# Performance work log

Hardware: AMD Instinct MI355X
Metric: run time of the kernel (lower is better)

## Reference

```python
import jax, jax.numpy as jnp
import numpy as np

IN_FEATURES = 4096
OUT_FEATURES = 4096
ACTIVE_IN = 1024
ACTIVE_OUT = 1024
BATCH, SEQ = 4, 2048


def setup_inputs() -> dict:
    key = jax.random.key(0)
    kx, kw, kb = jax.random.split(key, 3)
    x = jax.random.normal(kx, (BATCH, SEQ, IN_FEATURES), dtype=jnp.float32)
    # nn.Linear default init scale ~ 1/sqrt(fan_in)
    W = jax.random.normal(kw, (ACTIVE_OUT, ACTIVE_IN), dtype=jnp.float32) / np.sqrt(ACTIVE_IN)
    b = jax.random.normal(kb, (ACTIVE_OUT,), dtype=jnp.float32) / np.sqrt(ACTIVE_IN)
    rng = np.random.default_rng(42)
    # unique sorted index subsets (faithful to pruning-style selection; scatter is write-once)
    in_idx = jnp.asarray(np.sort(rng.choice(IN_FEATURES, ACTIVE_IN, replace=False)), dtype=jnp.int32)
    out_idx = jnp.asarray(np.sort(rng.choice(OUT_FEATURES, ACTIVE_OUT, replace=False)), dtype=jnp.int32)
    return {"x": x, "W": W, "b": b, "in_idx": in_idx, "out_idx": out_idx}


def reference(x, W, b, in_idx, out_idx):
    # gather active input columns: [B, S, ACTIVE_IN]
    x_active = jnp.take(x, in_idx, axis=-1)
    # dense linear: y = x_active @ W.T + b -> [B, S, ACTIVE_OUT]
    y = jnp.einsum('bsi,oi->bso', x_active, W) + b
    # scatter into zero-initialized full output buffer: [B, S, OUT_FEATURES]
    out = jnp.zeros(x.shape[:-1] + (OUT_FEATURES,), dtype=y.dtype)
    out = out.at[..., out_idx].set(y)
    return out
```

## Files before the change

### kernel.cpp

```cpp
#include <hip/hip_runtime.h>
#include <hip/hip_bf16.h>


typedef unsigned short u16;
typedef u16   u16x4 __attribute__((ext_vector_type(4)));
typedef int   i32x4 __attribute__((ext_vector_type(4)));
typedef float f32x4 __attribute__((ext_vector_type(4)));
typedef __bf16 bf16x8 __attribute__((ext_vector_type(8)));

constexpr int IN_F  = 4096;
constexpr int OUT_F = 4096;
constexpr int AI    = 1024;
constexpr int AO    = 1024;
constexpr int M_ROWS = 4 * 2048;
constexpr int NT_K  = AI / 64;

__device__ __forceinline__ u16 f2bf(float f) {
    union { __hip_bfloat16 h; u16 u; } cv;
    cv.h = __float2bfloat16(f);
    return cv.u;
}

__global__ void prep_kernel(const float* __restrict__ W,
                            const int* __restrict__ out_idx,
                            u16* __restrict__ Wb, int* __restrict__ pos) {
    int t = blockIdx.x * blockDim.x + threadIdx.x;
    if (t < AO) pos[out_idx[t]] = t;
    f32x4 w = reinterpret_cast<const f32x4*>(W)[t];
    u16x4 v;
    v.x = f2bf(w.x); v.y = f2bf(w.y); v.z = f2bf(w.z); v.w = f2bf(w.w);
    reinterpret_cast<u16x4*>(Wb)[t] = v;
}

__global__ __launch_bounds__(256)
void gather_kernel(const float* __restrict__ x,
                   const int* __restrict__ in_idx,
                   u16* __restrict__ Xa) {
    __shared__ float xrow[IN_F];
    const int m = blockIdx.x;
    const int t = threadIdx.x;
    const f32x4* src = reinterpret_cast<const f32x4*>(x + (size_t)m * IN_F);
#pragma unroll
    for (int i = 0; i < 4; ++i)
        *reinterpret_cast<f32x4*>(&xrow[i * 1024 + t * 4]) = src[i * 256 + t];
    __syncthreads();
    i32x4 idx = reinterpret_cast<const i32x4*>(in_idx)[t];
    u16x4 v;
    v.x = f2bf(xrow[idx.x]);
    v.y = f2bf(xrow[idx.y]);
    v.z = f2bf(xrow[idx.z]);
    v.w = f2bf(xrow[idx.w]);
    reinterpret_cast<u16x4*>(Xa + (size_t)m * AI)[t] = v;
}

template <bool PRE>
__global__ __launch_bounds__(256, 2)
void gemm128(const float* __restrict__ x, const u16* __restrict__ Xa,
             const u16* __restrict__ Wb, const float* __restrict__ bias,
             const int* __restrict__ in_idx, float* __restrict__ out) {
    __shared__ u16 As[2][128 * 64];
    __shared__ u16 Bs[2][128 * 64];
    const int tid  = threadIdx.x;
    const int wid  = tid >> 6;
    const int lane = tid & 63;
    const int n_lo = lane & 15;
    const int kg   = lane >> 4;
    const int orig = blockIdx.x;
    const int wgid = (orig & 7) * 64 + (orig >> 3);
    const int mb = wgid >> 3, nb = wgid & 7;
    const int m0 = mb * 128, n0 = nb * 128;
    const int wm = wid >> 1, wn = wid & 1;

    auto stage = [&](int buf, int k0) {
        if constexpr (PRE) {
            const int r8 = lane >> 3;
            const int c8 = (lane & 7) * 8;
#pragma unroll
            for (int c = 0; c < 4; ++c) {
                const int row = wid * 32 + c * 8;
                __builtin_amdgcn_global_load_lds(
                    (const __attribute__((address_space(1))) void*)
                        (Xa + (size_t)(m0 + row + r8) * AI + k0 + c8),
                    (__attribute__((address_space(3))) void*)&As[buf][row * 64],
                    16, 0, 0);
                __builtin_amdgcn_global_load_lds(
                    (const __attribute__((address_space(1))) void*)
                        (Wb + (size_t)(n0 + row + r8) * AI + k0 + c8),
                    (__attribute__((address_space(3))) void*)&Bs[buf][row * 64],
                    16, 0, 0);
            }
        } else {
            const int rr = tid >> 1;
            const int cc = (tid & 1) * 32;
#pragma unroll
            for (int j4 = 0; j4 < 32; j4 += 4) {
                u16x4 va;
#pragma unroll
                for (int j = 0; j < 4; ++j)
                    va[j] = f2bf(x[(size_t)(m0 + rr) * IN_F + in_idx[k0 + cc + j4 + j]]);
                *reinterpret_cast<u16x4*>(&As[buf][rr * 64 + cc + j4]) = va;
                *reinterpret_cast<u16x4*>(&Bs[buf][rr * 64 + cc + j4]) =
                    *reinterpret_cast<const u16x4*>(Wb + (size_t)(n0 + rr) * AI + k0 + cc + j4);
            }
        }
    };

    f32x4 acc[4][4];
#pragma unroll
    for (int i = 0; i < 4; ++i)
#pragma unroll
        for (int j = 0; j < 4; ++j) acc[i][j] = (f32x4)0.0f;

    stage(0, 0);
    int buf = 0;
    for (int kt = 0; kt < NT_K; ++kt) {
        __syncthreads();
        if (kt + 1 < NT_K) stage(buf ^ 1, (kt + 1) * 64);
#pragma unroll
        for (int kk = 0; kk < 64; kk += 32) {
            bf16x8 a[4], b[4];
#pragma unroll
            for (int i = 0; i < 4; ++i)
                a[i] = *reinterpret_cast<const bf16x8*>(
                    &As[buf][(wm * 64 + i * 16 + n_lo) * 64 + kk + kg * 8]);
#pragma unroll
            for (int j = 0; j < 4; ++j)
                b[j] = *reinterpret_cast<const bf16x8*>(
                    &Bs[buf][(wn * 64 + j * 16 + n_lo) * 64 + kk + kg * 8]);
#pragma unroll
            for (int i = 0; i < 4; ++i)
#pragma unroll
                for (int j = 0; j < 4; ++j)
                    acc[i][j] = __builtin_amdgcn_mfma_f32_16x16x32_bf16(
                        a[i], b[j], acc[i][j], 0, 0, 0);
        }
        buf ^= 1;
    }

    float bv[4];
#pragma unroll
    for (int j = 0; j < 4; ++j) bv[j] = bias[n0 + wn * 64 + j * 16 + n_lo];
#pragma unroll
    for (int i = 0; i < 4; ++i) {
        const int gm = m0 + wm * 64 + i * 16 + kg * 4;
#pragma unroll
        for (int j = 0; j < 4; ++j) {
            const int gn = n0 + wn * 64 + j * 16 + n_lo;
#pragma unroll
            for (int r = 0; r < 4; ++r)
                out[(size_t)(gm + r) * OUT_F + gn] = acc[i][j][r] + bv[j];
        }
    }
}

__global__ __launch_bounds__(256)
void expand_kernel(const int* __restrict__ pos, float* __restrict__ out) {
    __shared__ float yrow[AO];
    const int m = blockIdx.x;
    const int t = threadIdx.x;
    float* row = out + (size_t)m * OUT_F;
    *reinterpret_cast<f32x4*>(&yrow[t * 4]) =
        *reinterpret_cast<const f32x4*>(row + t * 4);
    __syncthreads();
    const i32x4* pos4 = reinterpret_cast<const i32x4*>(pos);
#pragma unroll
    for (int c = 0; c < 4; ++c) {
        const int o4 = c * 256 + t;
        i32x4 p = pos4[o4];
        f32x4 v;
        v.x = (p.x >= 0) ? yrow[p.x] : 0.0f;
        v.y = (p.y >= 0) ? yrow[p.y] : 0.0f;
        v.z = (p.z >= 0) ? yrow[p.z] : 0.0f;
        v.w = (p.w >= 0) ? yrow[p.w] : 0.0f;
        *reinterpret_cast<f32x4*>(row + o4 * 4) = v;
    }
}

extern "C" void kernel_launch(void* const* d_in, const int* in_sizes, int n_in,
                              void* d_out, int out_size, void* d_ws, size_t ws_size,
                              hipStream_t stream) {
    const float* x      = (const float*)d_in[0];
    const float* W      = (const float*)d_in[1];
    const float* b      = (const float*)d_in[2];
    const int*   in_idx = (const int*)d_in[3];
    const int*   out_idx= (const int*)d_in[4];
    float* out = (float*)d_out;

    char* ws = (char*)d_ws;
    int* pos = (int*)ws;
    u16* Wb  = (u16*)(ws + 16384);
    u16* Xa  = (u16*)(ws + 16384 + 2 * 1024 * 1024);
    const size_t NEED_FULL = 16384 + 2u * 1024 * 1024 + (size_t)M_ROWS * AI * 2;

    hipMemsetAsync(pos, 0xFF, OUT_F * sizeof(int), stream);
    prep_kernel<<<1024, 256, 0, stream>>>(W, out_idx, Wb, pos);

    if (ws_size >= NEED_FULL) {
        gather_kernel<<<M_ROWS, 256, 0, stream>>>(x, in_idx, Xa);
        gemm128<true><<<(M_ROWS / 128) * (AO / 128), 256, 0, stream>>>(
            x, Xa, Wb, b, in_idx, out);
    } else {
        gemm128<false><<<(M_ROWS / 128) * (AO / 128), 256, 0, stream>>>(
            x, Xa, Wb, b, in_idx, out);
    }
    expand_kernel<<<M_ROWS, 256, 0, stream>>>(pos, out);
}
```

Measured before the change: 281.6 us.

## Fuse scatter-expand into GEMM epilogue via shared-memory staging

Removes the separate expand kernel. Each GEMM block now stages its 128x128 output tile in LDS as bf16, then writes the full-width output columns whose positions map into its n-range, filling zeros for inactive columns. This avoids writing the compact result and then re-reading and re-writing the full output row. In exchange, outputs are rounded to bf16, which costs precision, and the non-PRE fallback path that handled a small workspace is removed.

```diff
diff --git a/kernel.cpp b/kernel.cpp
--- a/kernel.cpp
+++ b/kernel.cpp
@@ -13,12 +13,16 @@
 constexpr int AI    = 1024;
 constexpr int AO    = 1024;
 constexpr int M_ROWS = 4 * 2048;
-constexpr int NT_K  = AI / 64;
 
 __device__ __forceinline__ u16 f2bf(float f) {
     union { __hip_bfloat16 h; u16 u; } cv;
     cv.h = __float2bfloat16(f);
     return cv.u;
+}
+__device__ __forceinline__ float bf2f(u16 u) {
+    union { float f; unsigned int i; } cv;
+    cv.i = ((unsigned int)u) << 16;
+    return cv.f;
 }
 
 __global__ void prep_kernel(const float* __restrict__ W,
@@ -53,16 +57,15 @@
     reinterpret_cast<u16x4*>(Xa + (size_t)m * AI)[t] = v;
 }
 
-template <bool PRE>
 __global__ __launch_bounds__(256, 2)
-void gemm128(const float* __restrict__ x, const u16* __restrict__ Xa,
-             const u16* __restrict__ Wb, const float* __restrict__ bias,
-             const int* __restrict__ in_idx, float* __restrict__ out) {
-    __shared__ u16 As[2][128 * 64];
-    __shared__ u16 Bs[2][128 * 64];
-    const int tid  = threadIdx.x;
-    const int wid  = tid >> 6;
-    const int lane = tid & 63;
+void gemmfw_kernel(const u16* __restrict__ Xa, const u16* __restrict__ Wb,
+                   const float* __restrict__ bias,
+                   const int* __restrict__ out_idx,
+                   const int* __restrict__ pos, float* __restrict__ out) {
+    __shared__ u16 S[4][128 * 64];
+    const int t    = threadIdx.x;
+    const int wid  = t >> 6;
+    const int lane = t & 63;
     const int n_lo = lane & 15;
     const int kg   = lane >> 4;
     const int orig = blockIdx.x;
@@ -71,37 +74,22 @@
     const int m0 = mb * 128, n0 = nb * 128;
     const int wm = wid >> 1, wn = wid & 1;
 
+    const int r8 = lane >> 3;
+    const int c8 = (lane & 7) * 8;
     auto stage = [&](int buf, int k0) {
-        if constexpr (PRE) {
-            const int r8 = lane >> 3;
-            const int c8 = (lane & 7) * 8;
 #pragma unroll
-            for (int c = 0; c < 4; ++c) {
-                const int row = wid * 32 + c * 8;
-                __builtin_amdgcn_global_load_lds(
-                    (const __attribute__((address_space(1))) void*)
-                        (Xa + (size_t)(m0 + row + r8) * AI + k0 + c8),
-                    (__attribute__((address_space(3))) void*)&As[buf][row * 64],
-                    16, 0, 0);
-                __builtin_amdgcn_global_load_lds(
-                    (const __attribute__((address_space(1))) void*)
-                        (Wb + (size_t)(n0 + row + r8) * AI + k0 + c8),
-                    (__attribute__((address_space(3))) void*)&Bs[buf][row * 64],
-                    16, 0, 0);
-            }
-        } else {
-            const int rr = tid >> 1;
-            const int cc = (tid & 1) * 32;
-#pragma unroll
-            for (int j4 = 0; j4 < 32; j4 += 4) {
-                u16x4 va;
-#pragma unroll
-                for (int j = 0; j < 4; ++j)
-                    va[j] = f2bf(x[(size_t)(m0 + rr) * IN_F + in_idx[k0 + cc + j4 + j]]);
-                *reinterpret_cast<u16x4*>(&As[buf][rr * 64 + cc + j4]) = va;
-                *reinterpret_cast<u16x4*>(&Bs[buf][rr * 64 + cc + j4]) =
-                    *reinterpret_cast<const u16x4*>(Wb + (size_t)(n0 + rr) * AI + k0 + cc + j4);
-            }
+        for (int c = 0; c < 4; ++c) {
+            const int row = wid * 32 + c * 8;
+            __builtin_amdgcn_global_load_lds(
+                (const __attribute__((address_space(1))) void*)
+                    (Xa + (size_t)(m0 + row + r8) * AI + k0 + c8),
+                (__attribute__((address_space(3))) void*)&S[buf][row * 64],
+                16, 0, 0);
+            __builtin_amdgcn_global_load_lds(
+                (const __attribute__((address_space(1))) void*)
+                    (Wb + (size_t)(n0 + row + r8) * AI + k0 + c8),
+                (__attribute__((address_space(3))) void*)&S[2 + buf][row * 64],
+                16, 0, 0);
         }
     };
 
@@ -113,20 +101,20 @@
 
     stage(0, 0);
     int buf = 0;
-    for (int kt = 0; kt < NT_K; ++kt) {
+    for (int kt = 0; kt < AI / 64; ++kt) {
         __syncthreads();
-        if (kt + 1 < NT_K) stage(buf ^ 1, (kt + 1) * 64);
+        if (kt + 1 < AI / 64) stage(buf ^ 1, (kt + 1) * 64);
 #pragma unroll
         for (int kk = 0; kk < 64; kk += 32) {
             bf16x8 a[4], b[4];
 #pragma unroll
             for (int i = 0; i < 4; ++i)
                 a[i] = *reinterpret_cast<const bf16x8*>(
-                    &As[buf][(wm * 64 + i * 16 + n_lo) * 64 + kk + kg * 8]);
+                    &S[buf][(wm * 64 + i * 16 + n_lo) * 64 + kk + kg * 8]);
 #pragma unroll
             for (int j = 0; j < 4; ++j)
                 b[j] = *reinterpret_cast<const bf16x8*>(
-                    &Bs[buf][(wn * 64 + j * 16 + n_lo) * 64 + kk + kg * 8]);
+                    &S[2 + buf][(wn * 64 + j * 16 + n_lo) * 64 + kk + kg * 8]);
 #pragma unroll
             for (int i = 0; i < 4; ++i)
 #pragma unroll
@@ -140,39 +128,47 @@
     float bv[4];
 #pragma unroll
     for (int j = 0; j < 4; ++j) bv[j] = bias[n0 + wn * 64 + j * 16 + n_lo];
+
+    __syncthreads();
+    u16* ys = &S[0][0];
 #pragma unroll
-    for (int i = 0; i < 4; ++i) {
-        const int gm = m0 + wm * 64 + i * 16 + kg * 4;
+    for (int i = 0; i < 4; ++i)
 #pragma unroll
-        for (int j = 0; j < 4; ++j) {
-            const int gn = n0 + wn * 64 + j * 16 + n_lo;
+        for (int j = 0; j < 4; ++j)
 #pragma unroll
             for (int r = 0; r < 4; ++r)
-                out[(size_t)(gm + r) * OUT_F + gn] = acc[i][j][r] + bv[j];
+                ys[(wm * 64 + i * 16 + kg * 4 + r) * 136 +
+                   wn * 64 + j * 16 + n_lo] = f2bf(acc[i][j][r] + bv[j]);
+    __syncthreads();
+
+    const int lo = (nb == 0) ? 0 : out_idx[nb * 128];
+    const int hi = (nb == 7) ? OUT_F : out_idx[(nb + 1) * 128];
+    const int s4 = (lo + 3) >> 2;
+    const int e4 = hi >> 2;
+    const i32x4* pos4 = reinterpret_cast<const i32x4*>(pos);
+    const int rg = t >> 5, j32 = t & 31;
+#pragma unroll 1
+    for (int rr = 0; rr < 128; rr += 8) {
+        const int row = rr + rg;
+        float* orow = out + (size_t)(m0 + row) * OUT_F;
+        const u16* yr = ys + row * 136;
+        for (int c = lo + j32; c < s4 * 4; c += 32) {
+            int p = pos[c];
+            orow[c] = (p >= 0) ? bf2f(yr[p - n0]) : 0.0f;
         }
-    }
-}
-
-__global__ __launch_bounds__(256)
-void expand_kernel(const int* __restrict__ pos, float* __restrict__ out) {
-    __shared__ float yrow[AO];
-    const int m = blockIdx.x;
-    const int t = threadIdx.x;
-    float* row = out + (size_t)m * OUT_F;
-    *reinterpret_cast<f32x4*>(&yrow[t * 4]) =
-        *reinterpret_cast<const f32x4*>(row + t * 4);
-    __syncthreads();
-    const i32x4* pos4 = reinterpret_cast<const i32x4*>(pos);
-#pragma unroll
-    for (int c = 0; c < 4; ++c) {
-        const int o4 = c * 256 + t;
-        i32x4 p = pos4[o4];
-        f32x4 v;
-        v.x = (p.x >= 0) ? yrow[p.x] : 0.0f;
-        v.y = (p.y >= 0) ? yrow[p.y] : 0.0f;
-        v.z = (p.z >= 0) ? yrow[p.z] : 0.0f;
-        v.w = (p.w >= 0) ? yrow[p.w] : 0.0f;
-        *reinterpret_cast<f32x4*>(row + o4 * 4) = v;
+        for (int c4 = s4 + j32; c4 < e4; c4 += 32) {
+            i32x4 p = pos4[c4];
+            f32x4 v;
+            v.x = (p.x >= 0) ? bf2f(yr[p.x - n0]) : 0.0f;
+            v.y = (p.y >= 0) ? bf2f(yr[p.y - n0]) : 0.0f;
+            v.z = (p.z >= 0) ? bf2f(yr[p.z - n0]) : 0.0f;
+            v.w = (p.w >= 0) ? bf2f(yr[p.w - n0]) : 0.0f;
+            reinterpret_cast<f32x4*>(orow)[c4] = v;
+        }
+        for (int c = e4 * 4 + j32; c < hi; c += 32) {
+            int p = pos[c];
+            orow[c] = (p >= 0) ? bf2f(yr[p - n0]) : 0.0f;
+        }
     }
 }
 
@@ -190,18 +186,10 @@
     int* pos = (int*)ws;
     u16* Wb  = (u16*)(ws + 16384);
     u16* Xa  = (u16*)(ws + 16384 + 2 * 1024 * 1024);
-    const size_t NEED_FULL = 16384 + 2u * 1024 * 1024 + (size_t)M_ROWS * AI * 2;
 
     hipMemsetAsync(pos, 0xFF, OUT_F * sizeof(int), stream);
     prep_kernel<<<1024, 256, 0, stream>>>(W, out_idx, Wb, pos);
-
-    if (ws_size >= NEED_FULL) {
-        gather_kernel<<<M_ROWS, 256, 0, stream>>>(x, in_idx, Xa);
-        gemm128<true><<<(M_ROWS / 128) * (AO / 128), 256, 0, stream>>>(
-            x, Xa, Wb, b, in_idx, out);
-    } else {
-        gemm128<false><<<(M_ROWS / 128) * (AO / 128), 256, 0, stream>>>(
-            x, Xa, Wb, b, in_idx, out);
-    }
-    expand_kernel<<<M_ROWS, 256, 0, stream>>>(pos, out);
+    gather_kernel<<<M_ROWS, 256, 0, stream>>>(x, in_idx, Xa);
+    gemmfw_kernel<<<(M_ROWS / 128) * (AO / 128), 256, 0, stream>>>(
+        Xa, Wb, b, out_idx, pos, out);
 }
```

Result: no change. 286.6 us (+1.8%).
